# Kernel tuning notes

Hardware: AMD Instinct MI355X
Metric: run time of the kernel (lower is better)

## Reference

```python
import jax, jax.numpy as jnp
import numpy as np

N = 50000
D = 256
H = 128
L = 64
V = 3
E = 1600000
P = 10000


def setup_inputs() -> dict:
    key = jax.random.key(0)
    ks = jax.random.split(key, 10)
    X = jax.random.normal(ks[0], (N, D), dtype=jnp.float32)
    # row-normalize features, mimicking preprocess_features
    X = X / (jnp.sum(jnp.abs(X), axis=1, keepdims=True) + 1e-8)
    edge_idx = jax.random.randint(ks[1], (V, E, 2), 0, N, dtype=jnp.int32)
    edge_vals = jax.random.uniform(ks[2], (V, E), dtype=jnp.float32) / 32.0  # ~normalized adj weights
    W = jax.random.normal(ks[3], (V, D, H), dtype=jnp.float32) / np.sqrt(D)
    b = jnp.zeros((V, H), dtype=jnp.float32)
    Wmu = jax.random.normal(ks[4], (V * H, L), dtype=jnp.float32) / np.sqrt(V * H)
    bmu = jnp.zeros((L,), dtype=jnp.float32)
    Wsig = jax.random.normal(ks[5], (V * H, L), dtype=jnp.float32) / np.sqrt(V * H)
    bsig = jnp.zeros((L,), dtype=jnp.float32)
    pos_edges = jax.random.randint(ks[6], (P, 2), 0, N, dtype=jnp.int32)
    neg_edges = jax.random.randint(ks[7], (P, 2), 0, N, dtype=jnp.int32)
    return {"X": X, "edge_idx": edge_idx, "edge_vals": edge_vals, "W": W, "b": b,
            "Wmu": Wmu, "bmu": bmu, "Wsig": Wsig, "bsig": bsig,
            "pos_edges": pos_edges, "neg_edges": neg_edges}


def _energy_kl(mu, sigma, pairs):
    # pairs: [P,2]; KL(N_j || N_i) style energy as in graph2gauss
    mu_i = mu[pairs[:, 0]]          # [P,L]
    mu_j = mu[pairs[:, 1]]
    sig_i = sigma[pairs[:, 0]]
    sig_j = sigma[pairs[:, 1]]
    ratio = sig_j / sig_i           # [P,L]
    trace_fac = jnp.sum(ratio, axis=1)
    log_det = jnp.sum(jnp.log(ratio + 1e-14), axis=1)
    mu_diff_sq = jnp.sum(jnp.square(mu_i - mu_j) / sig_i, axis=1)
    return 0.5 * (trace_fac + mu_diff_sq - L - log_det)


def reference(X, edge_idx, edge_vals, W, b, Wmu, bmu, Wsig, bsig, pos_edges, neg_edges):
    # Per-view sparse GCN layer: relu(A_v @ (X @ W_v) + b_v)
    XW = jnp.einsum('nd,vdh->vnh', X, W)  # [V,N,H]

    def view_conv(xw, idx, vals, bv):
        src, dst = idx[:, 0], idx[:, 1]
        msgs = vals[:, None] * xw[src]                          # [E,H] gather
        agg = jax.ops.segment_sum(msgs, dst, num_segments=N)    # [N,H] scatter-add
        return jax.nn.relu(agg + bv)

    h = jax.vmap(view_conv)(XW, edge_idx, edge_vals, b)  # [V,N,H]
    # concat views along feature dim (reduce=None)
    concat = jnp.transpose(h, (1, 0, 2)).reshape(N, V * H)  # [N, V*H]

    # Gaussian encoder (non_linear=True): mu linear; sigma = elu(...) + 1 + eps > 0
    mu = concat @ Wmu + bmu
    sigma = jax.nn.elu(concat @ Wsig + bsig) + 1.0 + 1e-14

    eng_pos = _energy_kl(mu, sigma, pos_edges)
    eng_neg = _energy_kl(mu, sigma, neg_edges)
    energy = jnp.square(eng_pos) + jnp.exp(-eng_neg)
    return jnp.mean(energy)
```

## Files before the change

### kernel.cpp

```cpp
#include <hip/hip_runtime.h>
#include <hip/hip_fp16.h>

#define N_NODES 50000
#define DIM 256
#define HID 128
#define LAT 64
#define NV 3
#define NE 1600000
#define NP 10000
#define NBUCK 196
#define BIN_CHUNK 4096
#define BSTRIDE 12288
#define STAGE2 12288
#define EWAVES 1000

typedef short v8s __attribute__((ext_vector_type(8)));
typedef float v4f __attribute__((ext_vector_type(4)));
typedef float v2f __attribute__((ext_vector_type(2)));

__device__ __forceinline__ unsigned f2bf1(float f) {
  unsigned x = __float_as_uint(f);
  return (x + 0x7fffu + ((x >> 16) & 1u)) >> 16;
}
__device__ __forceinline__ unsigned pack2bf(float a, float b) {
  return (f2bf1(a) & 0xffffu) | (f2bf1(b) << 16);
}

__global__ __launch_bounds__(256) void k_wt(const float* __restrict__ W,
                                            const float* __restrict__ Wmu,
                                            const float* __restrict__ Wsig,
                                            unsigned short* __restrict__ WtA,
                                            unsigned short* __restrict__ Wt2) {
  int t = blockIdx.x * 256 + threadIdx.x;
  if (t < NV * HID * DIM) {
    int d = t & 255, vh = t >> 8;
    int h = vh & 127, v = vh >> 7;
    WtA[t] = (unsigned short)f2bf1(W[((size_t)v * DIM + d) * HID + h]);
  }
  int t2 = t - NV * HID * DIM;
  if (t2 >= 0 && t2 < HID * (NV * HID)) {
    int k = t2 % 384, o = t2 / 384;
    float w = (o < 64) ? Wmu[(size_t)k * 64 + o] : Wsig[(size_t)k * 64 + (o - 64)];
    Wt2[t2] = (unsigned short)f2bf1(w);
  }
}

#define BM1 32
__global__ __launch_bounds__(192) void k_gemm_xw(const float* __restrict__ X,
                                                 const unsigned short* __restrict__ WtA,
                                                 unsigned char* __restrict__ XW8) {
  const int nbase = blockIdx.x * BM1;
  const int tid = threadIdx.x;
  const int lane = tid & 63, wv = tid >> 6;
  __shared__ unsigned short Xs[BM1 * 256];
#pragma unroll
  for (int i = 0; i < 6; i++) {
    int task = i * 192 + tid;
    if (task < BM1 * 32) {
      int r = task >> 5, g = task & 31;
      int n = nbase + r;
      float4 x0 = make_float4(0.f, 0.f, 0.f, 0.f), x1 = x0;
      if (n < N_NODES) {
        const float4* xp = reinterpret_cast<const float4*>(X + (size_t)n * DIM + g * 8);
        x0 = xp[0]; x1 = xp[1];
      }
      int gp = g ^ (r & 7);
      uint4 u;
      u.x = pack2bf(x0.x, x0.y); u.y = pack2bf(x0.z, x0.w);
      u.z = pack2bf(x1.x, x1.y); u.w = pack2bf(x1.z, x1.w);
      *reinterpret_cast<uint4*>(&Xs[r * 256 + gp * 8]) = u;
    }
  }
  __syncthreads();
  const unsigned short* Wv = WtA + (size_t)wv * HID * DIM;
  const int bcol = lane & 15, bk = lane >> 4;
  v4f acc[2][8];
#pragma unroll
  for (int mt = 0; mt < 2; mt++)
#pragma unroll
    for (int nt = 0; nt < 8; nt++)
#pragma unroll
      for (int q = 0; q < 4; q++) acc[mt][nt][q] = 0.f;
  for (int ks = 0; ks < 8; ks++) {
    v8s B[8];
#pragma unroll
    for (int nt = 0; nt < 8; nt++)
      B[nt] = *reinterpret_cast<const v8s*>(Wv + (size_t)(nt * 16 + bcol) * DIM + ks * 32 + bk * 8);
#pragma unroll
    for (int mt = 0; mt < 2; mt++) {
      int r = mt * 16 + bcol;
      int g = ks * 4 + bk;
      v8s A = *reinterpret_cast<const v8s*>(&Xs[r * 256 + (g ^ (r & 7)) * 8]);
#pragma unroll
      for (int nt = 0; nt < 8; nt++)
        acc[mt][nt] = __builtin_amdgcn_mfma_f32_16x16x32_bf16(A, B[nt], acc[mt][nt], 0, 0, 0);
    }
  }
  unsigned char* out = XW8 + (size_t)wv * N_NODES * 128;
#pragma unroll
  for (int mt = 0; mt < 2; mt++)
#pragma unroll
    for (int rr = 0; rr < 4; rr++) {
      int n = nbase + mt * 16 + bk * 4 + rr;
      if (n < N_NODES) {
#pragma unroll
        for (int nt = 0; nt < 8; nt++) {
          int r8 = __builtin_amdgcn_cvt_pk_fp8_f32(acc[mt][nt][rr] * 64.f, 0.f, 0, false);
          out[(size_t)n * 128 + nt * 16 + bcol] = (unsigned char)(r8 & 0xff);
        }
      }
    }
}

__global__ __launch_bounds__(256) void k_bin(const int* __restrict__ edge_idx,
                                             const float* __restrict__ edge_vals,
                                             int* __restrict__ bcur,
                                             unsigned* __restrict__ spack4) {
  const int v = blockIdx.y;
  const int tid = threadIdx.x;
  const int lane = tid & 63, wv = tid >> 6;
  __shared__ unsigned buf[BIN_CHUNK];
  __shared__ unsigned short bid[BIN_CHUNK];
  __shared__ int lcount[NBUCK];
  __shared__ int loffs[NBUCK];
  __shared__ int gbase[NBUCK];
  __shared__ int wsum[4];
  if (tid < NBUCK) lcount[tid] = 0;
  __syncthreads();

  const int ebase = blockIdx.x * BIN_CHUNK;
  const int2* ei = reinterpret_cast<const int2*>(edge_idx) + (size_t)v * NE;
  const float* ev = edge_vals + (size_t)v * NE;

  unsigned px[16];
  int sdy[16];
  int rk[16];
#pragma unroll
  for (int i = 0; i < 16; i++) {
    int e = ebase + i * 256 + tid;
    bool ok = e < NE;
    int2 sd = ok ? ei[e] : make_int2(0, 0);
    float val = ok ? ev[e] : 0.f;
    int qv = (int)(val * 8192.f + 0.5f);
    qv = min(qv, 255);
    px[i] = (((unsigned)sd.x) << 16) | (((unsigned)qv) << 8) | ((unsigned)sd.y & 255u);
    sdy[i] = sd.y;
    rk[i] = ok ? atomicAdd(&lcount[sd.y >> 8], 1) : 0;
  }
  __syncthreads();
  {
    int c = (tid < NBUCK) ? lcount[tid] : 0;
    int s = c;
#pragma unroll
    for (int off = 1; off < 64; off <<= 1) {
      int t = __shfl_up(s, off);
      if (lane >= off) s += t;
    }
    if ((tid & 63) == 63) wsum[wv] = s;
    __syncthreads();
    int pre = 0;
#pragma unroll
    for (int w = 0; w < 4; w++) pre += (w < wv) ? wsum[w] : 0;
    if (tid < NBUCK) loffs[tid] = pre + s - c;
    __syncthreads();
    if (tid < NBUCK) gbase[tid] = atomicAdd(&bcur[v * NBUCK + tid], lcount[tid]);
  }
  __syncthreads();
#pragma unroll
  for (int i = 0; i < 16; i++) {
    int e = ebase + i * 256 + tid;
    if (e < NE) {
      int bkt = sdy[i] >> 8;
      int slot = loffs[bkt] + rk[i];
      buf[slot] = px[i];
      bid[slot] = (unsigned short)bkt;
    }
  }
  __syncthreads();
  const int total = loffs[NBUCK - 1] + lcount[NBUCK - 1];
  for (int s = tid; s < total; s += 256) {
    int bkt = bid[s];
    unsigned q = buf[s];
    spack4[(size_t)(v * NBUCK + bkt) * BSTRIDE + gbase[bkt] + (s - loffs[bkt])] = q;
  }
}

__global__ __launch_bounds__(1024) void k_sort2(const int* __restrict__ bcur,
                                                const unsigned* __restrict__ spack4,
                                                unsigned* __restrict__ csr,
                                                int* __restrict__ counts_g,
                                                int* __restrict__ offsets_g) {
  const int b = blockIdx.x, v = blockIdx.y;
  const int tid = threadIdx.x;
  __shared__ unsigned buf[STAGE2];
  __shared__ int h[256], cur[256];
  __shared__ int wsum[4];
  if (tid < 256) h[tid] = 0;
  __syncthreads();
  const int vb = v * NBUCK + b;
  const int cnt = bcur[vb];
  const size_t base = (size_t)vb * BSTRIDE;
  const unsigned* ep = spack4 + base;
  for (int i = tid; i < cnt; i += 1024) atomicAdd(&h[ep[i] & 0xffu], 1);
  __syncthreads();
  {
    const int lane = tid & 63, wv = tid >> 6;
    int c = (tid < 256) ? h[tid] : 0;
    int s = c;
#pragma unroll
    for (int off = 1; off < 64; off <<= 1) {
      int t = __shfl_up(s, off);
      if (lane >= off) s += t;
    }
    if (tid < 256 && lane == 63) wsum[wv] = s;
    __syncthreads();
    if (tid < 256) {
      int pre = 0;
#pragma unroll
      for (int w = 0; w < 4; w++) pre += (w < wv) ? wsum[w] : 0;
      int excl = pre + s - c;
      cur[tid] = excl;
      int n = (b << 8) + tid;
      if (n < N_NODES) {
        counts_g[v * N_NODES + n] = c;
        offsets_g[v * N_NODES + n] = (int)base + excl;
      }
    }
  }
  __syncthreads();
  for (int i = tid; i < cnt; i += 1024) {
    unsigned q = ep[i];
    int r = atomicAdd(&cur[q & 0xffu], 1);
    if (r < STAGE2) buf[r] = q;
  }
  __syncthreads();
  const int m = min(cnt, STAGE2);
  for (int s = tid; s < m; s += 1024) csr[base + s] = buf[s];
}

__global__ __launch_bounds__(256) void k_agg(const int* __restrict__ counts_g,
                                             const int* __restrict__ offsets_g,
                                             const unsigned* __restrict__ csr,
                                             const unsigned char* __restrict__ XW8,
                                             const float* __restrict__ b,
                                             unsigned* __restrict__ cat) {
  const int v = blockIdx.y;
  const int wave = threadIdx.x >> 6;
  const int lane = threadIdx.x & 63;
  const int half = lane >> 5;
  const int fl = lane & 31;
  const int n = blockIdx.x * 4 + wave;
  const int cnt = counts_g[v * N_NODES + n];
  const unsigned* pp = csr + offsets_g[v * N_NODES + n];
  const unsigned char* xwb = XW8 + (size_t)v * N_NODES * 128 + fl * 4;
  float a0 = 0.f, a1 = 0.f, a2 = 0.f, a3 = 0.f;
  int c0 = 0;
  for (; c0 + 16 <= cnt; c0 += 16) {
    unsigned pj[8], d[8];
#pragma unroll
    for (int s = 0; s < 8; s++) pj[s] = pp[c0 + 2 * s + half];
#pragma unroll
    for (int s = 0; s < 8; s++)
      d[s] = *reinterpret_cast<const unsigned*>(xwb + ((size_t)(pj[s] >> 16) << 7));
#pragma unroll
    for (int s = 0; s < 8; s++) {
      float qv = (float)((pj[s] >> 8) & 0xffu);
      v2f f0 = __builtin_amdgcn_cvt_pk_f32_fp8((int)d[s], false);
      v2f f1 = __builtin_amdgcn_cvt_pk_f32_fp8((int)d[s], true);
      a0 += qv * f0[0]; a1 += qv * f0[1];
      a2 += qv * f1[0]; a3 += qv * f1[1];
    }
  }
  if (c0 < cnt) {
#pragma unroll
    for (int s = 0; s < 8; s++) {
      int idx = c0 + 2 * s + half;
      unsigned pj = (idx < cnt) ? pp[idx] : 0u;
      unsigned d = *reinterpret_cast<const unsigned*>(xwb + ((size_t)(pj >> 16) << 7));
      float qv = (float)((pj >> 8) & 0xffu);
      v2f f0 = __builtin_amdgcn_cvt_pk_f32_fp8((int)d, false);
      v2f f1 = __builtin_amdgcn_cvt_pk_f32_fp8((int)d, true);
      a0 += qv * f0[0]; a1 += qv * f0[1];
      a2 += qv * f1[0]; a3 += qv * f1[1];
    }
  }
  a0 += __shfl_xor(a0, 32); a1 += __shfl_xor(a1, 32);
  a2 += __shfl_xor(a2, 32); a3 += __shfl_xor(a3, 32);
  if (half == 0) {
    const float4 bb = *reinterpret_cast<const float4*>(b + v * HID + fl * 4);
    const float sc = 1.f / 524288.f;
    float h0 = a0 * sc + bb.x, h1 = a1 * sc + bb.y;
    float h2 = a2 * sc + bb.z, h3 = a3 * sc + bb.w;
    h0 = h0 > 0.f ? h0 : 0.f; h1 = h1 > 0.f ? h1 : 0.f;
    h2 = h2 > 0.f ? h2 : 0.f; h3 = h3 > 0.f ? h3 : 0.f;
    uint2 o;
    o.x = pack2bf(h0, h1);
    o.y = pack2bf(h2, h3);
    *reinterpret_cast<uint2*>(cat + (size_t)n * 192 + v * 64 + fl * 2) = o;
  }
}

__global__ __launch_bounds__(256) void k_musig(const unsigned short* __restrict__ catus,
                                               const unsigned short* __restrict__ Wt2,
                                               const float* __restrict__ bmu,
                                               const float* __restrict__ bsig,
                                               float* __restrict__ mu,
                                               float* __restrict__ sig) {
  const int nbase = blockIdx.x * 64;
  const int tid = threadIdx.x;
  const int lane = tid & 63, wv = tid >> 6;
  __shared__ unsigned short Cs[64 * 384];
#pragma unroll
  for (int i = 0; i < 12; i++) {
    int task = i * 256 + tid;
    int r = task / 48, g = task % 48;
    int n = nbase + r;
    uint4 u = make_uint4(0u, 0u, 0u, 0u);
    if (n < N_NODES) u = *reinterpret_cast<const uint4*>(catus + (size_t)n * 384 + g * 8);
    int gp = (g & ~7) | ((g & 7) ^ (r & 7));
    *reinterpret_cast<uint4*>(&Cs[r * 384 + gp * 8]) = u;
  }
  __syncthreads();
  const int bcol = lane & 15, bk = lane >> 4;
  v4f acc[8];
#pragma unroll
  for (int nt = 0; nt < 8; nt++)
#pragma unroll
    for (int q = 0; q < 4; q++) acc[nt][q] = 0.f;
  for (int ks = 0; ks < 12; ks++) {
    v8s B[8];
#pragma unroll
    for (int nt = 0; nt < 8; nt++)
      B[nt] = *reinterpret_cast<const v8s*>(Wt2 + (size_t)(nt * 16 + bcol) * 384 + ks * 32 + bk * 8);
    int r = wv * 16 + bcol;
    int g = ks * 4 + bk;
    int gp = (g & ~7) | ((g & 7) ^ (r & 7));
    v8s A = *reinterpret_cast<const v8s*>(&Cs[r * 384 + gp * 8]);
#pragma unroll
    for (int nt = 0; nt < 8; nt++)
      acc[nt] = __builtin_amdgcn_mfma_f32_16x16x32_bf16(A, B[nt], acc[nt], 0, 0, 0);
  }
#pragma unroll
  for (int rr = 0; rr < 4; rr++) {
    int n = nbase + wv * 16 + bk * 4 + rr;
    if (n < N_NODES) {
#pragma unroll
      for (int nt = 0; nt < 8; nt++) {
        int o = nt * 16 + bcol;
        float val = acc[nt][rr];
        if (o < 64) {
          mu[(size_t)n * 64 + o] = val + bmu[o];
        } else {
          float s = val + bsig[o - 64];
          float e = (s > 0.f) ? s : (__expf(s) - 1.f);
          sig[(size_t)n * 64 + (o - 64)] = e + 1.f + 1e-14f;
        }
      }
    }
  }
}

__global__ __launch_bounds__(256) void k_energy1(const float* __restrict__ mu,
                                                 const float* __restrict__ sig,
                                                 const int* __restrict__ pos_e,
                                                 const int* __restrict__ neg_e,
                                                 float* __restrict__ partial) {
  const int lane = threadIdx.x & 63;
  const int gw = blockIdx.x * 4 + (threadIdx.x >> 6);
  float accum = 0.f;
  int t = gw;
  int2 pr = make_int2(0, 0);
  if (t < 2 * NP)
    pr = (t < NP) ? reinterpret_cast<const int2*>(pos_e)[t]
                  : reinterpret_cast<const int2*>(neg_e)[t - NP];
  for (; t < 2 * NP; t += EWAVES) {
    const bool ispos = t < NP;
    const int tn = t + EWAVES;
    int2 nxt = make_int2(0, 0);
    if (tn < 2 * NP)
      nxt = (tn < NP) ? reinterpret_cast<const int2*>(pos_e)[tn]
                      : reinterpret_cast<const int2*>(neg_e)[tn - NP];
    float mi = mu[(size_t)pr.x * 64 + lane], mj = mu[(size_t)pr.y * 64 + lane];
    float si = sig[(size_t)pr.x * 64 + lane], sj = sig[(size_t)pr.y * 64 + lane];
    float ratio = sj / si;
    float t1 = ratio;
    float t2 = __logf(ratio + 1e-14f);
    float d = mi - mj;
    float t3 = d * d / si;
#pragma unroll
    for (int off = 32; off; off >>= 1) {
      t1 += __shfl_xor(t1, off);
      t2 += __shfl_xor(t2, off);
      t3 += __shfl_xor(t3, off);
    }
    float eng = 0.5f * (t1 + t3 - 64.f - t2);
    accum += ispos ? (eng * eng) : __expf(-eng);
    pr = nxt;
  }
  if (lane == 0) partial[gw] = accum;
}

__global__ __launch_bounds__(256) void k_ered(const float* __restrict__ partial,
                                              float* __restrict__ out) {
  const int tid = threadIdx.x;
  const int lane = tid & 63, wv = tid >> 6;
  __shared__ float ws_[4];
  float s = 0.f;
  for (int i = tid; i < EWAVES; i += 256) s += partial[i];
#pragma unroll
  for (int off = 32; off; off >>= 1) s += __shfl_xor(s, off);
  if (lane == 0) ws_[wv] = s;
  __syncthreads();
  if (tid == 0) out[0] = (ws_[0] + ws_[1] + ws_[2] + ws_[3]) * (1.f / NP);
}

extern "C" void kernel_launch(void* const* d_in, const int* in_sizes, int n_in,
                              void* d_out, int out_size, void* d_ws, size_t ws_size,
                              hipStream_t stream) {
  const float* X = (const float*)d_in[0];
  const int* edge_idx = (const int*)d_in[1];
  const float* edge_vals = (const float*)d_in[2];
  const float* W = (const float*)d_in[3];
  const float* b = (const float*)d_in[4];
  const float* Wmu = (const float*)d_in[5];
  const float* bmu = (const float*)d_in[6];
  const float* Wsig = (const float*)d_in[7];
  const float* bsig = (const float*)d_in[8];
  const int* pos_e = (const int*)d_in[9];
  const int* neg_e = (const int*)d_in[10];
  float* out = (float*)d_out;

  char* ws = (char*)d_ws;
  const size_t o_xw   = 0;
  const size_t o_cat  = 19200000;
  const size_t o_sp   = 57600000;
  const size_t o_csr  = 86501376;
  const size_t o_cntg = 115402752;
  const size_t o_offg = 116002752;
  const size_t o_bcur = 116602752;
  const size_t o_wta  = 116608000;
  const size_t o_wt2  = 116804608;
  const size_t o_part = 116902912;
  const size_t total  = 116906912;
  const size_t o_mu   = o_sp;
  const size_t o_sig  = o_sp + 12800000;
  if (ws_size < total) return;

  unsigned char* XW8 = (unsigned char*)(ws + o_xw);
  unsigned* cat = (unsigned*)(ws + o_cat);
  unsigned short* catus = (unsigned short*)(ws + o_cat);
  unsigned* spack4 = (unsigned*)(ws + o_sp);
  unsigned* csr = (unsigned*)(ws + o_csr);
  int* counts_g = (int*)(ws + o_cntg);
  int* offsets_g = (int*)(ws + o_offg);
  int* bcur = (int*)(ws + o_bcur);
  unsigned short* WtA = (unsigned short*)(ws + o_wta);
  unsigned short* Wt2 = (unsigned short*)(ws + o_wt2);
  float* partial = (float*)(ws + o_part);
  float* mu = (float*)(ws + o_mu);
  float* sig = (float*)(ws + o_sig);

  hipMemsetAsync(bcur, 0, NV * NBUCK * sizeof(int), stream);

  hipLaunchKernelGGL(k_wt, dim3((NV * HID * DIM + HID * 384 + 255) / 256), dim3(256), 0,
                     stream, W, Wmu, Wsig, WtA, Wt2);
  hipLaunchKernelGGL(k_gemm_xw, dim3((N_NODES + BM1 - 1) / BM1), dim3(192), 0, stream,
                     X, WtA, XW8);
  hipLaunchKernelGGL(k_bin, dim3((NE + BIN_CHUNK - 1) / BIN_CHUNK, NV), dim3(256), 0,
                     stream, edge_idx, edge_vals, bcur, spack4);
  hipLaunchKernelGGL(k_sort2, dim3(NBUCK, NV), dim3(1024), 0, stream,
                     bcur, spack4, csr, counts_g, offsets_g);
  hipLaunchKernelGGL(k_agg, dim3(N_NODES / 4, NV), dim3(256), 0, stream,
                     counts_g, offsets_g, csr, XW8, b, cat);
  hipLaunchKernelGGL(k_musig, dim3((N_NODES + 63) / 64), dim3(256), 0, stream,
                     catus, Wt2, bmu, bsig, mu, sig);
  hipLaunchKernelGGL(k_energy1, dim3(EWAVES / 4), dim3(256), 0, stream,
                     mu, sig, pos_e, neg_e, partial);
  hipLaunchKernelGGL(k_ered, dim3(1), dim3(256), 0, stream, partial, out);
}
```

Before: 284.2 us.

## Merge XW GEMM and edge binning into one launch; fold final reduction into energy kernel

Combines the independent XW GEMM and edge-binning kernels into a single heterogeneous grid whose blocks branch by index, sharing a shared-memory union, so the two memory-bound and compute-bound phases can overlap on the GPU and one launch boundary is removed. The separate final-reduction kernel is replaced by a last-block-done pattern using an atomic counter and threadfence inside the energy kernel. This adds a 256-thread block shape for the GEMM with one idle wave and higher shared-memory footprint per block, which may lower occupancy for the GEMM blocks.

Result: slower. 312.0 us (+9.8%).

```diff
diff --git a/kernel.cpp b/kernel.cpp
--- a/kernel.cpp
+++ b/kernel.cpp
@@ -10,6 +10,10 @@
 #define NP 10000
 #define NBUCK 196
 #define BIN_CHUNK 4096
+#define NB_BINCH 391
+#define NB_BIN (NB_BINCH * NV)
+#define BM1 32
+#define NB_GEMM ((N_NODES + BM1 - 1) / BM1)
 #define BSTRIDE 12288
 #define STAGE2 12288
 #define EWAVES 1000
@@ -45,18 +49,90 @@
   }
 }
 
-#define BM1 32
-__global__ __launch_bounds__(192) void k_gemm_xw(const float* __restrict__ X,
-                                                 const unsigned short* __restrict__ WtA,
-                                                 unsigned char* __restrict__ XW8) {
-  const int nbase = blockIdx.x * BM1;
+__global__ __launch_bounds__(256) void k_gb(const float* __restrict__ X,
+                                            const unsigned short* __restrict__ WtA,
+                                            unsigned char* __restrict__ XW8,
+                                            const int* __restrict__ edge_idx,
+                                            const float* __restrict__ edge_vals,
+                                            int* __restrict__ bcur,
+                                            unsigned* __restrict__ spack4) {
+  union SmemU {
+    struct { unsigned short Xs[BM1 * 256]; } g;
+    struct {
+      unsigned buf[BIN_CHUNK];
+      unsigned short bid[BIN_CHUNK];
+      int lcount[NBUCK]; int loffs[NBUCK]; int gbase[NBUCK]; int wsum[4];
+    } b;
+  };
+  __shared__ SmemU sm;
+  const int bx = blockIdx.x;
   const int tid = threadIdx.x;
-  const int lane = tid & 63, wv = tid >> 6;
-  __shared__ unsigned short Xs[BM1 * 256];
-#pragma unroll
-  for (int i = 0; i < 6; i++) {
-    int task = i * 192 + tid;
-    if (task < BM1 * 32) {
+
+  if (bx < NB_BIN) {
+    const int v = bx / NB_BINCH;
+    const int lane = tid & 63, wvv = tid >> 6;
+    if (tid < NBUCK) sm.b.lcount[tid] = 0;
+    __syncthreads();
+    const int ebase = (bx % NB_BINCH) * BIN_CHUNK;
+    const int2* ei = reinterpret_cast<const int2*>(edge_idx) + (size_t)v * NE;
+    const float* ev = edge_vals + (size_t)v * NE;
+    unsigned px[16];
+    int sdy[16];
+    int rk[16];
+#pragma unroll
+    for (int i = 0; i < 16; i++) {
+      int e = ebase + i * 256 + tid;
+      bool ok = e < NE;
+      int2 sd = ok ? ei[e] : make_int2(0, 0);
+      float val = ok ? ev[e] : 0.f;
+      int qv = (int)(val * 8192.f + 0.5f);
+      qv = min(qv, 255);
+      px[i] = (((unsigned)sd.x) << 16) | (((unsigned)qv) << 8) | ((unsigned)sd.y & 255u);
+      sdy[i] = sd.y;
+      rk[i] = ok ? atomicAdd(&sm.b.lcount[sd.y >> 8], 1) : 0;
+    }
+    __syncthreads();
+    {
+      int c = (tid < NBUCK) ? sm.b.lcount[tid] : 0;
+      int s = c;
+#pragma unroll
+      for (int off = 1; off < 64; off <<= 1) {
+        int t = __shfl_up(s, off);
+        if (lane >= off) s += t;
+      }
+      if (lane == 63) sm.b.wsum[wvv] = s;
+      __syncthreads();
+      int pre = 0;
+#pragma unroll
+      for (int w = 0; w < 4; w++) pre += (w < wvv) ? sm.b.wsum[w] : 0;
+      if (tid < NBUCK) sm.b.loffs[tid] = pre + s - c;
+      __syncthreads();
+      if (tid < NBUCK) sm.b.gbase[tid] = atomicAdd(&bcur[v * NBUCK + tid], sm.b.lcount[tid]);
+    }
+    __syncthreads();
+#pragma unroll
+    for (int i = 0; i < 16; i++) {
+      int e = ebase + i * 256 + tid;
+      if (e < NE) {
+        int bkt = sdy[i] >> 8;
+        int slot = sm.b.loffs[bkt] + rk[i];
+        sm.b.buf[slot] = px[i];
+        sm.b.bid[slot] = (unsigned short)bkt;
+      }
+    }
+    __syncthreads();
+    const int total = sm.b.loffs[NBUCK - 1] + sm.b.lcount[NBUCK - 1];
+    for (int s = tid; s < total; s += 256) {
+      int bkt = sm.b.bid[s];
+      unsigned q = sm.b.buf[s];
+      spack4[(size_t)(v * NBUCK + bkt) * BSTRIDE + sm.b.gbase[bkt] + (s - sm.b.loffs[bkt])] = q;
+    }
+  } else {
+    const int nbase = (bx - NB_BIN) * BM1;
+    const int lane = tid & 63, wv = tid >> 6;
+#pragma unroll
+    for (int i = 0; i < 4; i++) {
+      int task = i * 256 + tid;
       int r = task >> 5, g = task & 31;
       int n = nbase + r;
       float4 x0 = make_float4(0.f, 0.f, 0.f, 0.f), x1 = x0;
@@ -68,120 +144,49 @@
       uint4 u;
       u.x = pack2bf(x0.x, x0.y); u.y = pack2bf(x0.z, x0.w);
       u.z = pack2bf(x1.x, x1.y); u.w = pack2bf(x1.z, x1.w);
-      *reinterpret_cast<uint4*>(&Xs[r * 256 + gp * 8]) = u;
-    }
-  }
-  __syncthreads();
-  const unsigned short* Wv = WtA + (size_t)wv * HID * DIM;
-  const int bcol = lane & 15, bk = lane >> 4;
-  v4f acc[2][8];
-#pragma unroll
-  for (int mt = 0; mt < 2; mt++)
-#pragma unroll
-    for (int nt = 0; nt < 8; nt++)
-#pragma unroll
-      for (int q = 0; q < 4; q++) acc[mt][nt][q] = 0.f;
-  for (int ks = 0; ks < 8; ks++) {
-    v8s B[8];
-#pragma unroll
-    for (int nt = 0; nt < 8; nt++)
-      B[nt] = *reinterpret_cast<const v8s*>(Wv + (size_t)(nt * 16 + bcol) * DIM + ks * 32 + bk * 8);
-#pragma unroll
-    for (int mt = 0; mt < 2; mt++) {
-      int r = mt * 16 + bcol;
-      int g = ks * 4 + bk;
-      v8s A = *reinterpret_cast<const v8s*>(&Xs[r * 256 + (g ^ (r & 7)) * 8]);
-#pragma unroll
-      for (int nt = 0; nt < 8; nt++)
-        acc[mt][nt] = __builtin_amdgcn_mfma_f32_16x16x32_bf16(A, B[nt], acc[mt][nt], 0, 0, 0);
-    }
-  }
-  unsigned char* out = XW8 + (size_t)wv * N_NODES * 128;
-#pragma unroll
-  for (int mt = 0; mt < 2; mt++)
-#pragma unroll
-    for (int rr = 0; rr < 4; rr++) {
-      int n = nbase + mt * 16 + bk * 4 + rr;
-      if (n < N_NODES) {
-#pragma unroll
-        for (int nt = 0; nt < 8; nt++) {
-          int r8 = __builtin_amdgcn_cvt_pk_fp8_f32(acc[mt][nt][rr] * 64.f, 0.f, 0, false);
-          out[(size_t)n * 128 + nt * 16 + bcol] = (unsigned char)(r8 & 0xff);
+      *reinterpret_cast<uint4*>(&sm.g.Xs[r * 256 + gp * 8]) = u;
+    }
+    __syncthreads();
+    if (wv < 3) {
+      const unsigned short* Wv = WtA + (size_t)wv * HID * DIM;
+      const int bcol = lane & 15, bk = lane >> 4;
+      v4f acc[2][8];
+#pragma unroll
+      for (int mt = 0; mt < 2; mt++)
+#pragma unroll
+        for (int nt = 0; nt < 8; nt++)
+#pragma unroll
+          for (int q = 0; q < 4; q++) acc[mt][nt][q] = 0.f;
+      for (int ks = 0; ks < 8; ks++) {
+        v8s B[8];
+#pragma unroll
+        for (int nt = 0; nt < 8; nt++)
+          B[nt] = *reinterpret_cast<const v8s*>(Wv + (size_t)(nt * 16 + bcol) * DIM + ks * 32 + bk * 8);
+#pragma unroll
+        for (int mt = 0; mt < 2; mt++) {
+          int r = mt * 16 + bcol;
+          int g = ks * 4 + bk;
+          v8s A = *reinterpret_cast<const v8s*>(&sm.g.Xs[r * 256 + (g ^ (r & 7)) * 8]);
+#pragma unroll
+          for (int nt = 0; nt < 8; nt++)
+            acc[mt][nt] = __builtin_amdgcn_mfma_f32_16x16x32_bf16(A, B[nt], acc[mt][nt], 0, 0, 0);
         }
       }
-    }
-}
-
-__global__ __launch_bounds__(256) void k_bin(const int* __restrict__ edge_idx,
-                                             const float* __restrict__ edge_vals,
-                                             int* __restrict__ bcur,
-                                             unsigned* __restrict__ spack4) {
-  const int v = blockIdx.y;
-  const int tid = threadIdx.x;
-  const int lane = tid & 63, wv = tid >> 6;
-  __shared__ unsigned buf[BIN_CHUNK];
-  __shared__ unsigned short bid[BIN_CHUNK];
-  __shared__ int lcount[NBUCK];
-  __shared__ int loffs[NBUCK];
-  __shared__ int gbase[NBUCK];
-  __shared__ int wsum[4];
-  if (tid < NBUCK) lcount[tid] = 0;
-  __syncthreads();
-
-  const int ebase = blockIdx.x * BIN_CHUNK;
-  const int2* ei = reinterpret_cast<const int2*>(edge_idx) + (size_t)v * NE;
-  const float* ev = edge_vals + (size_t)v * NE;
-
-  unsigned px[16];
-  int sdy[16];
-  int rk[16];
-#pragma unroll
-  for (int i = 0; i < 16; i++) {
-    int e = ebase + i * 256 + tid;
-    bool ok = e < NE;
-    int2 sd = ok ? ei[e] : make_int2(0, 0);
-    float val = ok ? ev[e] : 0.f;
-    int qv = (int)(val * 8192.f + 0.5f);
-    qv = min(qv, 255);
-    px[i] = (((unsigned)sd.x) << 16) | (((unsigned)qv) << 8) | ((unsigned)sd.y & 255u);
-    sdy[i] = sd.y;
-    rk[i] = ok ? atomicAdd(&lcount[sd.y >> 8], 1) : 0;
-  }
-  __syncthreads();
-  {
-    int c = (tid < NBUCK) ? lcount[tid] : 0;
-    int s = c;
-#pragma unroll
-    for (int off = 1; off < 64; off <<= 1) {
-      int t = __shfl_up(s, off);
-      if (lane >= off) s += t;
-    }
-    if ((tid & 63) == 63) wsum[wv] = s;
-    __syncthreads();
-    int pre = 0;
-#pragma unroll
-    for (int w = 0; w < 4; w++) pre += (w < wv) ? wsum[w] : 0;
-    if (tid < NBUCK) loffs[tid] = pre + s - c;
-    __syncthreads();
-    if (tid < NBUCK) gbase[tid] = atomicAdd(&bcur[v * NBUCK + tid], lcount[tid]);
-  }
-  __syncthreads();
-#pragma unroll
-  for (int i = 0; i < 16; i++) {
-    int e = ebase + i * 256 + tid;
-    if (e < NE) {
-      int bkt = sdy[i] >> 8;
-      int slot = loffs[bkt] + rk[i];
-      buf[slot] = px[i];
-      bid[slot] = (unsigned short)bkt;
-    }
-  }
-  __syncthreads();
-  const int total = loffs[NBUCK - 1] + lcount[NBUCK - 1];
-  for (int s = tid; s < total; s += 256) {
-    int bkt = bid[s];
-    unsigned q = buf[s];
-    spack4[(size_t)(v * NBUCK + bkt) * BSTRIDE + gbase[bkt] + (s - loffs[bkt])] = q;
+      unsigned char* out = XW8 + (size_t)wv * N_NODES * 128;
+#pragma unroll
+      for (int mt = 0; mt < 2; mt++)
+#pragma unroll
+        for (int rr = 0; rr < 4; rr++) {
+          int n = nbase + mt * 16 + bk * 4 + rr;
+          if (n < N_NODES) {
+#pragma unroll
+            for (int nt = 0; nt < 8; nt++) {
+              int r8 = __builtin_amdgcn_cvt_pk_fp8_f32(acc[mt][nt][rr] * 64.f, 0.f, 0, false);
+              out[(size_t)n * 128 + nt * 16 + bcol] = (unsigned char)(r8 & 0xff);
+            }
+          }
+        }
+    }
   }
 }
 
@@ -364,9 +369,12 @@
                                                  const float* __restrict__ sig,
                                                  const int* __restrict__ pos_e,
                                                  const int* __restrict__ neg_e,
-                                                 float* __restrict__ partial) {
-  const int lane = threadIdx.x & 63;
-  const int gw = blockIdx.x * 4 + (threadIdx.x >> 6);
+                                                 float* __restrict__ partial,
+                                                 int* __restrict__ done,
+                                                 float* __restrict__ out) {
+  const int tid = threadIdx.x;
+  const int lane = tid & 63;
+  const int gw = blockIdx.x * 4 + (tid >> 6);
   float accum = 0.f;
   int t = gw;
   int2 pr = make_int2(0, 0);
@@ -398,20 +406,21 @@
     pr = nxt;
   }
   if (lane == 0) partial[gw] = accum;
-}
-
-__global__ __launch_bounds__(256) void k_ered(const float* __restrict__ partial,
-                                              float* __restrict__ out) {
-  const int tid = threadIdx.x;
-  const int lane = tid & 63, wv = tid >> 6;
-  __shared__ float ws_[4];
-  float s = 0.f;
-  for (int i = tid; i < EWAVES; i += 256) s += partial[i];
-#pragma unroll
-  for (int off = 32; off; off >>= 1) s += __shfl_xor(s, off);
-  if (lane == 0) ws_[wv] = s;
-  __syncthreads();
-  if (tid == 0) out[0] = (ws_[0] + ws_[1] + ws_[2] + ws_[3]) * (1.f / NP);
+  __threadfence();
+  __syncthreads();
+  __shared__ int lastflag;
+  __shared__ float wsum2[4];
+  if (tid == 0) lastflag = (atomicAdd(done, 1) == (int)gridDim.x - 1) ? 1 : 0;
+  __syncthreads();
+  if (lastflag) {
+    float s = 0.f;
+    for (int i = tid; i < EWAVES; i += 256) s += partial[i];
+#pragma unroll
+    for (int off = 32; off; off >>= 1) s += __shfl_xor(s, off);
+    if (lane == 0) wsum2[tid >> 6] = s;
+    __syncthreads();
+    if (tid == 0) out[0] = (wsum2[0] + wsum2[1] + wsum2[2] + wsum2[3]) * (1.f / NP);
+  }
 }
 
 extern "C" void kernel_launch(void* const* d_in, const int* in_sizes, int n_in,
@@ -438,10 +447,10 @@
   const size_t o_cntg = 115402752;
   const size_t o_offg = 116002752;
   const size_t o_bcur = 116602752;
-  const size_t o_wta  = 116608000;
-  const size_t o_wt2  = 116804608;
-  const size_t o_part = 116902912;
-  const size_t total  = 116906912;
+  const size_t o_wta  = 116605120;
+  const size_t o_wt2  = 116801728;
+  const size_t o_part = 116900032;
+  const size_t total  = 116904032;
   const size_t o_mu   = o_sp;
   const size_t o_sig  = o_sp + 12800000;
   if (ws_size < total) return;
@@ -454,20 +463,19 @@
   int* counts_g = (int*)(ws + o_cntg);
   int* offsets_g = (int*)(ws + o_offg);
   int* bcur = (int*)(ws + o_bcur);
+  int* done = bcur + NV * NBUCK;
   unsigned short* WtA = (unsigned short*)(ws + o_wta);
   unsigned short* Wt2 = (unsigned short*)(ws + o_wt2);
   float* partial = (float*)(ws + o_part);
   float* mu = (float*)(ws + o_mu);
   float* sig = (float*)(ws + o_sig);
 
-  hipMemsetAsync(bcur, 0, NV * NBUCK * sizeof(int), stream);
+  hipMemsetAsync(bcur, 0, (NV * NBUCK + 1) * sizeof(int), stream);
 
   hipLaunchKernelGGL(k_wt, dim3((NV * HID * DIM + HID * 384 + 255) / 256), dim3(256), 0,
                      stream, W, Wmu, Wsig, WtA, Wt2);
-  hipLaunchKernelGGL(k_gemm_xw, dim3((N_NODES + BM1 - 1) / BM1), dim3(192), 0, stream,
-                     X, WtA, XW8);
-  hipLaunchKernelGGL(k_bin, dim3((NE + BIN_CHUNK - 1) / BIN_CHUNK, NV), dim3(256), 0,
-                     stream, edge_idx, edge_vals, bcur, spack4);
+  hipLaunchKernelGGL(k_gb, dim3(NB_BIN + NB_GEMM), dim3(256), 0, stream,
+                     X, WtA, XW8, edge_idx, edge_vals, bcur, spack4);
   hipLaunchKernelGGL(k_sort2, dim3(NBUCK, NV), dim3(1024), 0, stream,
                      bcur, spack4, csr, counts_g, offsets_g);
   hipLaunchKernelGGL(k_agg, dim3(N_NODES / 4, NV), dim3(256), 0, stream,
@@ -475,6 +483,5 @@
   hipLaunchKernelGGL(k_musig, dim3((N_NODES + 63) / 64), dim3(256), 0, stream,
                      catus, Wt2, bmu, bsig, mu, sig);
   hipLaunchKernelGGL(k_energy1, dim3(EWAVES / 4), dim3(256), 0, stream,
-                     mu, sig, pos_e, neg_e, partial);
-  hipLaunchKernelGGL(k_ered, dim3(1), dim3(256), 0, stream, partial, out);
-}
+                     mu, sig, pos_e, neg_e, partial, done, out);
+}
```
